# Performance work log

Hardware: AMD Instinct MI355X
Metric: run time of the kernel (lower is better)

Reference implementation:

```python
import math
import jax, jax.numpy as jnp
import numpy as np

B, T, C = 4, 2048, 1024
NH, HD = 16, C // 16
FF = 4096
EPS = 1e-5


def _layernorm(x, g, b):
    mu = jnp.mean(x, axis=-1, keepdims=True)
    var = jnp.mean(jnp.square(x - mu), axis=-1, keepdims=True)
    return (x - mu) * jax.lax.rsqrt(var + EPS) * g + b


def _new_gelu(x):
    c = math.sqrt(2.0 / math.pi)
    return 0.5 * x * (1.0 + jnp.tanh(c * (x + 0.044715 * x * x * x)))


def setup_inputs() -> dict:
    key = jax.random.key(0)
    ks = jax.random.split(key, 5)
    s = lambda fan_in: 1.0 / math.sqrt(fan_in)
    return {
        "x": jax.random.normal(ks[0], (B, T, C), jnp.float32),
        "ln1_g": jnp.ones((C,), jnp.float32),
        "ln1_b": jnp.zeros((C,), jnp.float32),
        "w_qkv": jax.random.normal(ks[1], (C, 3 * C), jnp.float32) * s(C),
        "b_qkv": jnp.zeros((3 * C,), jnp.float32),
        "w_attn_proj": jax.random.normal(ks[2], (C, C), jnp.float32) * s(C),
        "b_attn_proj": jnp.zeros((C,), jnp.float32),
        "ln2_g": jnp.ones((C,), jnp.float32),
        "ln2_b": jnp.zeros((C,), jnp.float32),
        "w_fc": jax.random.normal(ks[3], (C, FF), jnp.float32) * s(C),
        "b_fc": jnp.zeros((FF,), jnp.float32),
        "w_mlp_proj": jax.random.normal(ks[4], (FF, C), jnp.float32) * s(FF),
        "b_mlp_proj": jnp.zeros((C,), jnp.float32),
    }


def reference(x, ln1_g, ln1_b, w_qkv, b_qkv, w_attn_proj, b_attn_proj,
              ln2_g, ln2_b, w_fc, b_fc, w_mlp_proj, b_mlp_proj):
    # --- attention branch ---
    h = _layernorm(x, ln1_g, ln1_b)
    qkv = h @ w_qkv + b_qkv                      # [B,T,3C]
    q, k, v = jnp.split(qkv, 3, axis=-1)
    # [B,T,C] -> [B,NH,T,HD]
    to_heads = lambda t: t.reshape(B, T, NH, HD).transpose(0, 2, 1, 3)
    q, k, v = to_heads(q), to_heads(k), to_heads(v)
    scores = jnp.einsum("bhqd,bhkd->bhqk", q, k) / math.sqrt(HD)  # [B,NH,T,T]
    causal = jnp.tril(jnp.ones((T, T), bool))
    scores = jnp.where(causal, scores, -jnp.inf)
    probs = jax.nn.softmax(scores, axis=-1)
    attn = jnp.einsum("bhqk,bhkd->bhqd", probs, v)  # [B,NH,T,HD]
    attn = attn.transpose(0, 2, 1, 3).reshape(B, T, C)
    x = x + attn @ w_attn_proj + b_attn_proj
    # --- MLP branch ---
    h = _layernorm(x, ln2_g, ln2_b)
    h = _new_gelu(h @ w_fc + b_fc)
    x = x + h @ w_mlp_proj + b_mlp_proj
    return x
```

## Files before the change

kernel.cpp:

```cpp
#include <hip/hip_runtime.h>
#include <hip/hip_bf16.h>

typedef __bf16 bf16x8 __attribute__((ext_vector_type(8)));
typedef __bf16 bf16x4 __attribute__((ext_vector_type(4)));
typedef float f32x4 __attribute__((ext_vector_type(4)));

#define BM 128
#define BN 128
#define BK 32

__device__ __forceinline__ void gload16(const __bf16* g, __bf16* l) {
    __builtin_amdgcn_global_load_lds((const __attribute__((address_space(1))) void*)g,
                                     (__attribute__((address_space(3))) void*)l, 16, 0, 0);
}

__device__ __forceinline__ float gelu_f(float v) {
    float z = 0.7978845608028654f * (v + 0.044715f * v * v * v);
    float e = __expf(2.f * z);
    return 0.5f * v * (2.f - 2.f / (e + 1.f));
}

__device__ __forceinline__ int xcd_swizzle(int flat, int nwg) {
    return (flat & 7) * (nwg >> 3) + (flat >> 3);
}

__global__ __launch_bounds__(256) void diag_kernel(float* out, int n, float v) {
    int i = blockIdx.x * 256 + threadIdx.x;
    if (i < n) out[i] = v;
}

__global__ __launch_bounds__(256) void cvtT_kernel(
    const float* __restrict__ in, __bf16* __restrict__ out, int K, int N)
{
    __shared__ __bf16 tile[32][33];
    int bx = blockIdx.x * 32, by = blockIdx.y * 32;
    int tx = threadIdx.x & 31, ty = threadIdx.x >> 5;
#pragma unroll
    for (int i = 0; i < 32; i += 8)
        tile[ty + i][tx] = (__bf16)in[(size_t)(by + ty + i) * N + bx + tx];
    __syncthreads();
#pragma unroll
    for (int i = 0; i < 32; i += 8)
        out[(size_t)(bx + ty + i) * K + by + tx] = tile[tx][ty + i];
}

__global__ __launch_bounds__(256) void ln_kernel(
    const float* __restrict__ x, const float* __restrict__ g,
    const float* __restrict__ bta, __bf16* __restrict__ out)
{
    const int row = blockIdx.x, t = threadIdx.x;
    const float* xr = x + (size_t)row * 1024;
    float4 xv = ((const float4*)xr)[t];
    float f[4] = {xv.x, xv.y, xv.z, xv.w};
    float s = f[0] + f[1] + f[2] + f[3];
    float ss = f[0]*f[0] + f[1]*f[1] + f[2]*f[2] + f[3]*f[3];
#pragma unroll
    for (int off = 32; off; off >>= 1) {
        s  += __shfl_xor(s, off, 64);
        ss += __shfl_xor(ss, off, 64);
    }
    __shared__ float red[8];
    int lane = t & 63, w = t >> 6;
    if (lane == 0) { red[w] = s; red[4 + w] = ss; }
    __syncthreads();
    s  = red[0] + red[1] + red[2] + red[3];
    ss = red[4] + red[5] + red[6] + red[7];
    float mu = s * (1.f / 1024.f);
    float var = ss * (1.f / 1024.f) - mu * mu;
    float rstd = rsqrtf(fmaxf(var, 0.f) + 1e-5f);
    float4 gv = ((const float4*)g)[t];
    float4 bv = ((const float4*)bta)[t];
    bf16x4 ov;
    ov[0] = (__bf16)((f[0] - mu) * rstd * gv.x + bv.x);
    ov[1] = (__bf16)((f[1] - mu) * rstd * gv.y + bv.y);
    ov[2] = (__bf16)((f[2] - mu) * rstd * gv.z + bv.z);
    ov[3] = (__bf16)((f[3] - mu) * rstd * gv.w + bv.w);
    ((bf16x4*)(out + (size_t)row * 1024))[t] = ov;
}

template <int EPI>
__global__ __launch_bounds__(512, 2) void gemm256_kernel(
    const __bf16* __restrict__ A, const __bf16* __restrict__ BT,
    const float* __restrict__ bias, void* __restrict__ Cp, int M, int N, int K)
{
    __shared__ __align__(16) __bf16 lA[2][256 * 64];
    __shared__ __align__(16) __bf16 lB[2][256 * 64];
    const int t = threadIdx.x;
    const int lane = t & 63, w = t >> 6;
    const int wm = w >> 2, wn = w & 3;
    const int q4 = lane >> 4, r16 = lane & 15;
    const int nwg = gridDim.x * gridDim.y;
    const int nf = xcd_swizzle(blockIdx.y * gridDim.x + blockIdx.x, nwg);
    const int bm = (nf / gridDim.x) * 256, bn = (nf % gridDim.x) * 256;

    const int srow = t & 255;
    const int skc  = t >> 8;
    const __bf16* gA = A  + (size_t)(bm + srow) * K + skc * 8;
    const __bf16* gB = BT + (size_t)(bn + srow) * K + skc * 8;
    const int dst = skc * 2048 + srow * 8;

    f32x4 acc[8][4];
    f32x4 zero4 = {0.f, 0.f, 0.f, 0.f};
#pragma unroll
    for (int mi = 0; mi < 8; ++mi)
#pragma unroll
        for (int ni = 0; ni < 4; ++ni) acc[mi][ni] = zero4;

#pragma unroll
    for (int j = 0; j < 4; ++j) gload16(gA + j * 16, &lA[0][dst + j * 4096]);
#pragma unroll
    for (int j = 0; j < 4; ++j) gload16(gB + j * 16, &lB[0][dst + j * 4096]);
#pragma unroll
    for (int j = 0; j < 4; ++j) gload16(gA + 64 + j * 16, &lA[1][dst + j * 4096]);
    asm volatile("s_waitcnt vmcnt(4)" ::: "memory");
    __builtin_amdgcn_s_barrier();

    const int nt = K / 64;
    for (int ti = 0; ti < nt; ++ti) {
        const int p = ti & 1;
        bf16x8 af[4][2], bfr[2][2];
#pragma unroll
        for (int q = 0; q < 4; ++q) {
            const int qm = q >> 1, qn = q & 1;
            if (qn == 0) {
#pragma unroll
                for (int mi = 0; mi < 4; ++mi)
#pragma unroll
                    for (int ks = 0; ks < 2; ++ks)
                        af[mi][ks] = *(const bf16x8*)&lA[p][(ks * 4 + q4) * 2048 +
                            (wm * 128 + qm * 64 + mi * 16 + r16) * 8];
            }
#pragma unroll
            for (int ni = 0; ni < 2; ++ni)
#pragma unroll
                for (int ks = 0; ks < 2; ++ks)
                    bfr[ni][ks] = *(const bf16x8*)&lB[p][(ks * 4 + q4) * 2048 +
                        (wn * 64 + qn * 32 + ni * 16 + r16) * 8];
            if (q == 0 && ti + 1 < nt) {
                gload16(gB + (ti + 1) * 64,      &lB[p ^ 1][dst]);
                gload16(gB + (ti + 1) * 64 + 16, &lB[p ^ 1][dst + 4096]);
            }
            if (q == 1 && ti + 1 < nt) {
                gload16(gB + (ti + 1) * 64 + 32, &lB[p ^ 1][dst + 8192]);
                gload16(gB + (ti + 1) * 64 + 48, &lB[p ^ 1][dst + 12288]);
            }
            if (q == 3) {
                if (ti + 2 < nt) {
#pragma unroll
                    for (int j = 0; j < 4; ++j)
                        gload16(gA + (ti + 2) * 64 + j * 16, &lA[p][dst + j * 4096]);
                    asm volatile("s_waitcnt vmcnt(4)" ::: "memory");
                } else {
                    asm volatile("s_waitcnt vmcnt(0)" ::: "memory");
                }
            }
            __builtin_amdgcn_s_barrier();
            asm volatile("s_waitcnt lgkmcnt(0)" ::: "memory");
            __builtin_amdgcn_sched_barrier(0);
            __builtin_amdgcn_s_setprio(1);
#pragma unroll
            for (int mi = 0; mi < 4; ++mi)
#pragma unroll
                for (int ni = 0; ni < 2; ++ni) {
                    f32x4 v = acc[qm * 4 + mi][qn * 2 + ni];
                    v = __builtin_amdgcn_mfma_f32_16x16x32_bf16(af[mi][0], bfr[ni][0], v, 0, 0, 0);
                    v = __builtin_amdgcn_mfma_f32_16x16x32_bf16(af[mi][1], bfr[ni][1], v, 0, 0, 0);
                    acc[qm * 4 + mi][qn * 2 + ni] = v;
                }
            __builtin_amdgcn_s_setprio(0);
            __builtin_amdgcn_sched_barrier(0);
            __builtin_amdgcn_s_barrier();
        }
    }

#pragma unroll
    for (int mi = 0; mi < 8; ++mi) {
#pragma unroll
        for (int ni = 0; ni < 4; ++ni) {
#pragma unroll
            for (int i = 0; i < 4; ++i) {
                int r = bm + wm * 128 + mi * 16 + q4 * 4 + i;
                int c = bn + wn * 64 + ni * 16 + r16;
                float v = acc[mi][ni][i] + bias[c];
                if (EPI == 2) v = gelu_f(v);
                ((__bf16*)Cp)[(size_t)r * N + c] = (__bf16)v;
            }
        }
    }
}

template <int EPI, bool OUT32>
__global__ __launch_bounds__(256, 4) void gemm_bt_kernel(
    const __bf16* __restrict__ A, const __bf16* __restrict__ BT,
    const float* __restrict__ bias, const float* __restrict__ res,
    void* __restrict__ Cp, int M, int N, int K)
{
    __shared__ __align__(16) __bf16 lA[2][BM * BK];
    __shared__ __align__(16) __bf16 lB[2][BN * BK];
    const int t = threadIdx.x;
    const int lane = t & 63;
    const int wave = t >> 6;
    const int wm = wave >> 1, wn = wave & 1;
    const int q4 = lane >> 4, r16 = lane & 15;
    const int nwg = gridDim.x * gridDim.y;
    const int nf = xcd_swizzle(blockIdx.y * gridDim.x + blockIdx.x, nwg);
    const int bm = (nf / gridDim.x) * BM, bn = (nf % gridDim.x) * BN;

    const int srow = t & 127;
    const int skc = t >> 7;
    const __bf16* ga0 = A + (size_t)(bm + srow) * K + skc * 8;
    const __bf16* ga1 = ga0 + 16;
    const __bf16* gb0 = BT + (size_t)(bn + srow) * K + skc * 8;
    const __bf16* gb1 = gb0 + 16;

    f32x4 acc[4][4];
    f32x4 zero4 = {0.f, 0.f, 0.f, 0.f};
#pragma unroll
    for (int mi = 0; mi < 4; ++mi)
#pragma unroll
        for (int ni = 0; ni < 4; ++ni) acc[mi][ni] = zero4;

    gload16(ga0, &lA[0][t * 8]);
    gload16(ga1, &lA[0][t * 8 + 2048]);
    gload16(gb0, &lB[0][t * 8]);
    gload16(gb1, &lB[0][t * 8 + 2048]);
    ga0 += BK; ga1 += BK; gb0 += BK; gb1 += BK;
    __syncthreads();

    const int nk = K / BK;
    int cur = 0;
    for (int it = 0; it < nk; ++it) {
        if (it + 1 < nk) {
            gload16(ga0, &lA[cur ^ 1][t * 8]);
            gload16(ga1, &lA[cur ^ 1][t * 8 + 2048]);
            gload16(gb0, &lB[cur ^ 1][t * 8]);
            gload16(gb1, &lB[cur ^ 1][t * 8 + 2048]);
            ga0 += BK; ga1 += BK; gb0 += BK; gb1 += BK;
        }
        bf16x8 af[4], bfr[4];
#pragma unroll
        for (int i = 0; i < 4; ++i)
            af[i] = *(const bf16x8*)&lA[cur][q4 * 1024 + (wm * 64 + i * 16 + r16) * 8];
#pragma unroll
        for (int i = 0; i < 4; ++i)
            bfr[i] = *(const bf16x8*)&lB[cur][q4 * 1024 + (wn * 64 + i * 16 + r16) * 8];
#pragma unroll
        for (int mi = 0; mi < 4; ++mi)
#pragma unroll
            for (int ni = 0; ni < 4; ++ni)
                acc[mi][ni] = __builtin_amdgcn_mfma_f32_16x16x32_bf16(
                    af[mi], bfr[ni], acc[mi][ni], 0, 0, 0);
        if (it + 1 < nk) __syncthreads();
        cur ^= 1;
    }

#pragma unroll
    for (int mi = 0; mi < 4; ++mi) {
#pragma unroll
        for (int ni = 0; ni < 4; ++ni) {
#pragma unroll
            for (int i = 0; i < 4; ++i) {
                int r = bm + wm * 64 + mi * 16 + q4 * 4 + i;
                int c = bn + wn * 64 + ni * 16 + r16;
                float v = acc[mi][ni][i] + bias[c];
                if (EPI == 1) v += res[(size_t)r * N + c];
                if (EPI == 2) v = gelu_f(v);
                if (OUT32) ((float*)Cp)[(size_t)r * N + c] = v;
                else       ((__bf16*)Cp)[(size_t)r * N + c] = (__bf16)v;
            }
        }
    }
}

__global__ __launch_bounds__(256, 4) void attn_kernel(
    const __bf16* __restrict__ qkv, __bf16* __restrict__ attnb)
{
    __shared__ __align__(16) __bf16 lK[8192];
    __shared__ __align__(16) __bf16 lV[8192];
    __shared__ __align__(16) __bf16 lP[4][512];

    const int t = threadIdx.x, lane = t & 63, w = t >> 6;
    const int q4 = lane >> 4, r16 = lane & 15;
    const int nf = xcd_swizzle(blockIdx.y * 16 + blockIdx.x, 1024);
    const int qt = nf & 15;
    const int bh = nf >> 4;
    const int b = bh >> 4, h = bh & 15;
    const int qb = qt * 128;
    const __bf16* Qb = qkv + (size_t)b * 2048 * 3072 + h * 64;
    const __bf16* Kb = Qb + 1024;
    const __bf16* Vb = Qb + 2048;

    bf16x8 qf[2][2];
#pragma unroll
    for (int p = 0; p < 2; ++p) {
        int qrow = qb + p * 64 + w * 16 + r16;
        qf[p][0] = *(const bf16x8*)(Qb + (size_t)qrow * 3072 + q4 * 8);
        qf[p][1] = *(const bf16x8*)(Qb + (size_t)qrow * 3072 + 32 + q4 * 8);
#pragma unroll
        for (int j = 0; j < 8; ++j) {
            qf[p][0][j] = (__bf16)((float)qf[p][0][j] * 0.125f);
            qf[p][1][j] = (__bf16)((float)qf[p][1][j] * 0.125f);
        }
    }

    f32x4 zero4 = {0.f, 0.f, 0.f, 0.f};
    f32x4 o[2][4];
    float rs[2][4];
#pragma unroll
    for (int p = 0; p < 2; ++p)
#pragma unroll
        for (int i = 0; i < 4; ++i) { o[p][i] = zero4; rs[p][i] = 0.f; }

    const int skey = t & 127;
    const int vkc = t >> 6, svd = t & 63;

    for (int kb = 0; kb < qb + 128; kb += 128) {
        __syncthreads();
#pragma unroll
        for (int c = 0; c < 4; ++c)
            gload16(Kb + (size_t)(kb + skey) * 3072 + (c * 2 + (t >> 7)) * 8,
                    &lK[c * 2048 + t * 8]);
#pragma unroll
        for (int c = 0; c < 4; ++c) {
            int kc = c * 4 + vkc;
            bf16x8 vt;
#pragma unroll
            for (int j = 0; j < 8; ++j)
                vt[j] = Vb[(size_t)(kb + kc * 8 + j) * 3072 + svd];
            *(bf16x8*)&lV[kc * 512 + svd * 8] = vt;
        }
        __syncthreads();

#pragma unroll
        for (int p = 0; p < 2; ++p) {
            const int row0 = qb + p * 64 + w * 16 + q4 * 4;
            const bool interior = (kb + 127) <= (qb + p * 64 + w * 16);

            f32x4 s[8];
#pragma unroll
            for (int kg = 0; kg < 8; ++kg) {
                bf16x8 kfA = *(const bf16x8*)&lK[q4 * 1024 + (kg * 16 + r16) * 8];
                bf16x8 kfB = *(const bf16x8*)&lK[(4 + q4) * 1024 + (kg * 16 + r16) * 8];
                s[kg] = __builtin_amdgcn_mfma_f32_16x16x32_bf16(qf[p][0], kfA, zero4, 0, 0, 0);
                s[kg] = __builtin_amdgcn_mfma_f32_16x16x32_bf16(qf[p][1], kfB, s[kg], 0, 0, 0);
            }

#pragma unroll
            for (int kg = 0; kg < 8; ++kg)
#pragma unroll
                for (int i = 0; i < 4; ++i) {
                    float e = __expf(fminf(s[kg][i], 75.f));
                    if (!interior && (kb + kg * 16 + r16) > (row0 + i)) e = 0.f;
                    s[kg][i] = e;
                    rs[p][i] += e;
                }

#pragma unroll
            for (int c = 0; c < 4; ++c) {
#pragma unroll
                for (int kh = 0; kh < 2; ++kh)
#pragma unroll
                    for (int i = 0; i < 4; ++i)
                        lP[w][(kh * 2 + (r16 >> 3)) * 128 + (q4 * 4 + i) * 8 + (r16 & 7)] =
                            (__bf16)s[c * 2 + kh][i];
                asm volatile("s_waitcnt lgkmcnt(0)" ::: "memory");
                bf16x8 pf = *(const bf16x8*)&lP[w][q4 * 128 + r16 * 8];
#pragma unroll
                for (int ci = 0; ci < 4; ++ci) {
                    bf16x8 vf = *(const bf16x8*)&lV[(c * 4 + q4) * 512 + (ci * 16 + r16) * 8];
                    o[p][ci] = __builtin_amdgcn_mfma_f32_16x16x32_bf16(pf, vf, o[p][ci], 0, 0, 0);
                }
            }
        }
    }

#pragma unroll
    for (int p = 0; p < 2; ++p) {
#pragma unroll
        for (int off = 8; off; off >>= 1)
#pragma unroll
            for (int i = 0; i < 4; ++i) rs[p][i] += __shfl_xor(rs[p][i], off, 64);
#pragma unroll
        for (int ci = 0; ci < 4; ++ci)
#pragma unroll
            for (int i = 0; i < 4; ++i) {
                int trow = qb + p * 64 + w * 16 + q4 * 4 + i;
                float inv_l = (rs[p][i] > 0.f) ? (1.f / rs[p][i]) : 0.f;
                attnb[(size_t)(b * 2048 + trow) * 1024 + h * 64 + ci * 16 + r16] =
                    (__bf16)(o[p][ci][i] * inv_l);
            }
    }
}

extern "C" void kernel_launch(void* const* d_in, const int* in_sizes, int n_in,
                              void* d_out, int out_size, void* d_ws, size_t ws_size,
                              hipStream_t stream)
{
    const float* x      = (const float*)d_in[0];
    const float* ln1_g  = (const float*)d_in[1];
    const float* ln1_b  = (const float*)d_in[2];
    const float* w_qkv  = (const float*)d_in[3];
    const float* b_qkv  = (const float*)d_in[4];
    const float* w_proj = (const float*)d_in[5];
    const float* b_proj = (const float*)d_in[6];
    const float* ln2_g  = (const float*)d_in[7];
    const float* ln2_b  = (const float*)d_in[8];
    const float* w_fc   = (const float*)d_in[9];
    const float* b_fc   = (const float*)d_in[10];
    const float* w_mlp  = (const float*)d_in[11];
    const float* b_mlp  = (const float*)d_in[12];
    float* out = (float*)d_out;

    const size_t MiB = (size_t)1 << 20;
    if (ws_size < 136 * MiB) {
        float v = 1000.f + (float)(ws_size >> 20);
        diag_kernel<<<(out_size + 255) / 256, 256, 0, stream>>>(out, out_size, v);
        return;
    }

    char* ws = (char*)d_ws;
    __bf16* bufA   = (__bf16*)(ws);
    __bf16* bufB   = (__bf16*)(ws + 16 * MiB);
    float*  x1     = (float*) (ws + 80 * MiB);
    __bf16* wqkvT  = (__bf16*)(ws + 112 * MiB);
    __bf16* wprojT = (__bf16*)(ws + 118 * MiB);
    __bf16* wfcT   = (__bf16*)(ws + 120 * MiB);
    __bf16* wmlpT  = (__bf16*)(ws + 128 * MiB);

    cvtT_kernel<<<dim3(96, 32),  256, 0, stream>>>(w_qkv,  wqkvT,  1024, 3072);
    cvtT_kernel<<<dim3(32, 32),  256, 0, stream>>>(w_proj, wprojT, 1024, 1024);
    cvtT_kernel<<<dim3(128, 32), 256, 0, stream>>>(w_fc,   wfcT,   1024, 4096);
    cvtT_kernel<<<dim3(32, 128), 256, 0, stream>>>(w_mlp,  wmlpT,  4096, 1024);

    ln_kernel<<<8192, 256, 0, stream>>>(x, ln1_g, ln1_b, bufA);
    gemm256_kernel<0><<<dim3(12, 32), 512, 0, stream>>>(
        bufA, wqkvT, b_qkv, bufB, 8192, 3072, 1024);
    attn_kernel<<<dim3(16, 64), 256, 0, stream>>>(bufB, bufA);
    gemm_bt_kernel<1, true><<<dim3(8, 64), 256, 0, stream>>>(
        bufA, wprojT, b_proj, x, x1, 8192, 1024, 1024);
    ln_kernel<<<8192, 256, 0, stream>>>(x1, ln2_g, ln2_b, bufA);
    gemm256_kernel<2><<<dim3(16, 32), 512, 0, stream>>>(
        bufA, wfcT, b_fc, bufB, 8192, 4096, 1024);
    gemm_bt_kernel<1, true><<<dim3(8, 64), 256, 0, stream>>>(
        bufB, wmlpT, b_mlp, x1, out, 8192, 1024, 4096);
}
```

Baseline: 686.8 us.

## Replace 128x128 residual GEMM with 128x256 tile and interleaved prefetch pipeline

The two N=1024 residual GEMMs (attention projection and MLP down-projection) now use a new 512-thread kernel with 128x256 tiles and BK=64. B-tile loads for the next K step are spread across the four compute quarters, and A is prefetched two steps ahead, with explicit vmcnt waits, barriers and MFMA priority boosting. The larger tile raises reuse per byte loaded and the staggered loads aim to hide global latency behind MFMAs. The cost is 256 workgroups on the device instead of 512, which lowers occupancy and wave parallelism.

After: 680.1 us. Within noise of the previous version (-1.0%).

```diff
diff --git a/kernel.cpp b/kernel.cpp
--- a/kernel.cpp
+++ b/kernel.cpp
@@ -4,10 +4,6 @@
 typedef __bf16 bf16x8 __attribute__((ext_vector_type(8)));
 typedef __bf16 bf16x4 __attribute__((ext_vector_type(4)));
 typedef float f32x4 __attribute__((ext_vector_type(4)));
-
-#define BM 128
-#define BN 128
-#define BK 32
 
 __device__ __forceinline__ void gload16(const __bf16* g, __bf16* l) {
     __builtin_amdgcn_global_load_lds((const __attribute__((address_space(1))) void*)g,
@@ -189,29 +185,28 @@
     }
 }
 
-template <int EPI, bool OUT32>
-__global__ __launch_bounds__(256, 4) void gemm_bt_kernel(
+template <int EPI>
+__global__ __launch_bounds__(512, 2) void gemm128x256_kernel(
     const __bf16* __restrict__ A, const __bf16* __restrict__ BT,
     const float* __restrict__ bias, const float* __restrict__ res,
-    void* __restrict__ Cp, int M, int N, int K)
-{
-    __shared__ __align__(16) __bf16 lA[2][BM * BK];
-    __shared__ __align__(16) __bf16 lB[2][BN * BK];
+    float* __restrict__ C, int M, int N, int K)
+{
+    __shared__ __align__(16) __bf16 lA[2][128 * 64];
+    __shared__ __align__(16) __bf16 lB[2][256 * 64];
     const int t = threadIdx.x;
-    const int lane = t & 63;
-    const int wave = t >> 6;
-    const int wm = wave >> 1, wn = wave & 1;
+    const int lane = t & 63, w = t >> 6;
+    const int wm = w >> 2, wn = w & 3;
     const int q4 = lane >> 4, r16 = lane & 15;
     const int nwg = gridDim.x * gridDim.y;
     const int nf = xcd_swizzle(blockIdx.y * gridDim.x + blockIdx.x, nwg);
-    const int bm = (nf / gridDim.x) * BM, bn = (nf % gridDim.x) * BN;
-
-    const int srow = t & 127;
-    const int skc = t >> 7;
-    const __bf16* ga0 = A + (size_t)(bm + srow) * K + skc * 8;
-    const __bf16* ga1 = ga0 + 16;
-    const __bf16* gb0 = BT + (size_t)(bn + srow) * K + skc * 8;
-    const __bf16* gb1 = gb0 + 16;
+    const int bm = (nf / gridDim.x) * 128, bn = (nf % gridDim.x) * 256;
+
+    const int srA = t & 127, kqA = t >> 7;
+    const __bf16* gA = A + (size_t)(bm + srA) * K + kqA * 8;
+    const int dstA = kqA * 1024 + srA * 8;
+    const int srB = t & 255, skB = t >> 8;
+    const __bf16* gB = BT + (size_t)(bn + srB) * K + skB * 8;
+    const int dstB = skB * 2048 + srB * 8;
 
     f32x4 acc[4][4];
     f32x4 zero4 = {0.f, 0.f, 0.f, 0.f};
@@ -220,38 +215,71 @@
 #pragma unroll
         for (int ni = 0; ni < 4; ++ni) acc[mi][ni] = zero4;
 
-    gload16(ga0, &lA[0][t * 8]);
-    gload16(ga1, &lA[0][t * 8 + 2048]);
-    gload16(gb0, &lB[0][t * 8]);
-    gload16(gb1, &lB[0][t * 8 + 2048]);
-    ga0 += BK; ga1 += BK; gb0 += BK; gb1 += BK;
-    __syncthreads();
-
-    const int nk = K / BK;
-    int cur = 0;
-    for (int it = 0; it < nk; ++it) {
-        if (it + 1 < nk) {
-            gload16(ga0, &lA[cur ^ 1][t * 8]);
-            gload16(ga1, &lA[cur ^ 1][t * 8 + 2048]);
-            gload16(gb0, &lB[cur ^ 1][t * 8]);
-            gload16(gb1, &lB[cur ^ 1][t * 8 + 2048]);
-            ga0 += BK; ga1 += BK; gb0 += BK; gb1 += BK;
-        }
-        bf16x8 af[4], bfr[4];
-#pragma unroll
-        for (int i = 0; i < 4; ++i)
-            af[i] = *(const bf16x8*)&lA[cur][q4 * 1024 + (wm * 64 + i * 16 + r16) * 8];
-#pragma unroll
-        for (int i = 0; i < 4; ++i)
-            bfr[i] = *(const bf16x8*)&lB[cur][q4 * 1024 + (wn * 64 + i * 16 + r16) * 8];
-#pragma unroll
-        for (int mi = 0; mi < 4; ++mi)
-#pragma unroll
-            for (int ni = 0; ni < 4; ++ni)
-                acc[mi][ni] = __builtin_amdgcn_mfma_f32_16x16x32_bf16(
-                    af[mi], bfr[ni], acc[mi][ni], 0, 0, 0);
-        if (it + 1 < nk) __syncthreads();
-        cur ^= 1;
+#pragma unroll
+    for (int j = 0; j < 2; ++j) gload16(gA + j * 32, &lA[0][dstA + j * 4096]);
+#pragma unroll
+    for (int j = 0; j < 4; ++j) gload16(gB + j * 16, &lB[0][dstB + j * 4096]);
+#pragma unroll
+    for (int j = 0; j < 2; ++j) gload16(gA + 64 + j * 32, &lA[1][dstA + j * 4096]);
+    asm volatile("s_waitcnt vmcnt(2)" ::: "memory");
+    __builtin_amdgcn_s_barrier();
+
+    const int nt = K / 64;
+    for (int ti = 0; ti < nt; ++ti) {
+        const int p = ti & 1;
+        bf16x8 af[2][2], bfr[2][2];
+#pragma unroll
+        for (int q = 0; q < 4; ++q) {
+            const int qm = q >> 1, qn = q & 1;
+            if (qn == 0) {
+#pragma unroll
+                for (int mi = 0; mi < 2; ++mi)
+#pragma unroll
+                    for (int ks = 0; ks < 2; ++ks)
+                        af[mi][ks] = *(const bf16x8*)&lA[p][(ks * 4 + q4) * 1024 +
+                            (wm * 64 + qm * 32 + mi * 16 + r16) * 8];
+            }
+#pragma unroll
+            for (int ni = 0; ni < 2; ++ni)
+#pragma unroll
+                for (int ks = 0; ks < 2; ++ks)
+                    bfr[ni][ks] = *(const bf16x8*)&lB[p][(ks * 4 + q4) * 2048 +
+                        (wn * 64 + qn * 32 + ni * 16 + r16) * 8];
+            if (q == 0 && ti + 1 < nt) {
+                gload16(gB + (ti + 1) * 64,      &lB[p ^ 1][dstB]);
+                gload16(gB + (ti + 1) * 64 + 16, &lB[p ^ 1][dstB + 4096]);
+            }
+            if (q == 1 && ti + 1 < nt) {
+                gload16(gB + (ti + 1) * 64 + 32, &lB[p ^ 1][dstB + 8192]);
+                gload16(gB + (ti + 1) * 64 + 48, &lB[p ^ 1][dstB + 12288]);
+            }
+            if (q == 3) {
+                if (ti + 2 < nt) {
+#pragma unroll
+                    for (int j = 0; j < 2; ++j)
+                        gload16(gA + (ti + 2) * 64 + j * 32, &lA[p][dstA + j * 4096]);
+                    asm volatile("s_waitcnt vmcnt(2)" ::: "memory");
+                } else {
+                    asm volatile("s_waitcnt vmcnt(0)" ::: "memory");
+                }
+            }
+            __builtin_amdgcn_s_barrier();
+            asm volatile("s_waitcnt lgkmcnt(0)" ::: "memory");
+            __builtin_amdgcn_sched_barrier(0);
+            __builtin_amdgcn_s_setprio(1);
+#pragma unroll
+            for (int mi = 0; mi < 2; ++mi)
+#pragma unroll
+                for (int ni = 0; ni < 2; ++ni) {
+                    f32x4 v = acc[qm * 2 + mi][qn * 2 + ni];
+                    v = __builtin_amdgcn_mfma_f32_16x16x32_bf16(af[mi][0], bfr[ni][0], v, 0, 0, 0);
+                    v = __builtin_amdgcn_mfma_f32_16x16x32_bf16(af[mi][1], bfr[ni][1], v, 0, 0, 0);
+                    acc[qm * 2 + mi][qn * 2 + ni] = v;
+                }
+            __builtin_amdgcn_s_setprio(0);
+            __builtin_amdgcn_sched_barrier(0);
+            __builtin_amdgcn_s_barrier();
+        }
     }
 
 #pragma unroll
@@ -264,9 +292,7 @@
                 int c = bn + wn * 64 + ni * 16 + r16;
                 float v = acc[mi][ni][i] + bias[c];
                 if (EPI == 1) v += res[(size_t)r * N + c];
-                if (EPI == 2) v = gelu_f(v);
-                if (OUT32) ((float*)Cp)[(size_t)r * N + c] = v;
-                else       ((__bf16*)Cp)[(size_t)r * N + c] = (__bf16)v;
+                C[(size_t)r * N + c] = v;
             }
         }
     }
@@ -436,11 +462,11 @@
     gemm256_kernel<0><<<dim3(12, 32), 512, 0, stream>>>(
         bufA, wqkvT, b_qkv, bufB, 8192, 3072, 1024);
     attn_kernel<<<dim3(16, 64), 256, 0, stream>>>(bufB, bufA);
-    gemm_bt_kernel<1, true><<<dim3(8, 64), 256, 0, stream>>>(
+    gemm128x256_kernel<1><<<dim3(4, 64), 512, 0, stream>>>(
         bufA, wprojT, b_proj, x, x1, 8192, 1024, 1024);
     ln_kernel<<<8192, 256, 0, stream>>>(x1, ln2_g, ln2_b, bufA);
     gemm256_kernel<2><<<dim3(16, 32), 512, 0, stream>>>(
         bufA, wfcT, b_fc, bufB, 8192, 4096, 1024);
-    gemm_bt_kernel<1, true><<<dim3(8, 64), 256, 0, stream>>>(
+    gemm128x256_kernel<1><<<dim3(4, 64), 512, 0, stream>>>(
         bufB, wmlpT, b_mlp, x1, out, 8192, 1024, 4096);
 }
```
